# Optimization experiments

Measured on AMD Instinct MI355X. Metric: run time of the kernel, lower is better.

## Reference

```python
import jax, jax.numpy as jnp
import numpy as np

B, T, NLAT, N, D = 8, 4, 64, 2048, 1024
HEADS, HEAD_DIM = 16, 64
ADIM = HEADS * HEAD_DIM
EPS = 1e-5


def layer_norm(x, w, b):
    mu = jnp.mean(x, axis=-1, keepdims=True)
    var = jnp.var(x, axis=-1, keepdims=True)
    return (x - mu) * jax.lax.rsqrt(var + EPS) * w + b


def setup_inputs() -> dict:
    key = jax.random.key(0)
    ks = jax.random.split(key, 8)
    s = 0.02
    return {
        "latents": jax.random.normal(ks[0], (B, T, NLAT, D), jnp.float32),
        "x": jax.random.normal(ks[1], (B, T, N, D), jnp.float32),
        "Wq": jax.random.normal(ks[2], (D, ADIM), jnp.float32) * s,     # [in, out]
        "Wkv": jax.random.normal(ks[3], (D, 2 * ADIM), jnp.float32) * s,
        "Wout": jax.random.normal(ks[4], (ADIM, D), jnp.float32) * s,
        "bout": jnp.zeros((D,), jnp.float32),
        "lnl_w": jnp.ones((D,), jnp.float32),
        "lnl_b": jnp.zeros((D,), jnp.float32),
        "lnm_w": jnp.ones((D,), jnp.float32),
        "lnm_b": jnp.zeros((D,), jnp.float32),
    }


def reference(latents, x, Wq, Wkv, Wout, bout, lnl_w, lnl_b, lnm_w, lnm_b):
    scale = HEAD_DIM ** (-0.5)
    lat = layer_norm(latents, lnl_w, lnl_b)          # [B,T,NLAT,D]
    med = layer_norm(x, lnm_w, lnm_b)                # [B,T,N,D]
    q = lat @ Wq                                      # [B,T,NLAT,ADIM]
    kv_in = jnp.concatenate((med, lat), axis=-2)      # [B,T,N+NLAT,D]
    kv = kv_in @ Wkv                                  # [B,T,N+NLAT,2*ADIM]
    k, v = jnp.split(kv, 2, axis=-1)
    # split heads: b t n (h d) -> b h t n d
    def split_heads(z):
        b, t, n, _ = z.shape
        return z.reshape(b, t, n, HEADS, HEAD_DIM).transpose(0, 3, 1, 2, 4)
    q = split_heads(q) * scale
    k = split_heads(k)
    v = split_heads(v)
    scores = jnp.einsum('bhtid,bhtjd->bhtij', q, k)   # [B,H,T,NLAT,N+NLAT]
    attn = jax.nn.softmax(scores, axis=-1)            # max-subtract handled internally
    out = jnp.einsum('bhtij,bhtjd->bhtid', attn, v)   # [B,H,T,NLAT,HEAD_DIM]
    out = out.transpose(0, 2, 3, 1, 4).reshape(B, T, NLAT, ADIM)
    return out @ Wout + bout
```

## Files before the change

### kernel.cpp

```cpp
#include <hip/hip_runtime.h>
#include <hip/hip_bf16.h>
#include <stdint.h>

#define B_    8
#define T_    4
#define NLAT  64
#define NMED  2048
#define NKV   2112
#define D_    1024
#define HEADS 16
#define HD    64
#define ADIM  1024
#define BT    32

#define GK    1024
#define GN    2048
#define MT256 264

typedef __attribute__((ext_vector_type(8))) short bf16x8;
typedef __attribute__((ext_vector_type(4))) float f32x4;

__device__ __forceinline__ ushort f2bf(float f) {
  union { float f; uint32_t u; } v; v.f = f;
  return (ushort)((v.u + 0x7fff + ((v.u >> 16) & 1)) >> 16);
}

__device__ __forceinline__ void gload_lds16(const void* g, void* l) {
  __builtin_amdgcn_global_load_lds(
      (const __attribute__((address_space(1))) void*)g,
      (__attribute__((address_space(3))) void*)l, 16, 0, 0);
}

__device__ __forceinline__ f32x4 mfma16(bf16x8 a, bf16x8 b, f32x4 c) {
  return __builtin_amdgcn_mfma_f32_16x16x32_bf16(a, b, c, 0, 0, 0);
}

__global__ __launch_bounds__(256) void wtrans(const float* __restrict__ src,
                                              ushort* __restrict__ dst,
                                              int K, int Nm) {
  __shared__ float t[64][65];
  const int tr = blockIdx.y, tc = blockIdx.x;
  const int c = threadIdx.x & 63;
  const int r4 = threadIdx.x >> 6;
#pragma unroll
  for (int rr = 0; rr < 16; ++rr) {
    int r = r4 + rr * 4;
    t[r][c] = src[(size_t)(tr * 64 + r) * Nm + tc * 64 + c];
  }
  __syncthreads();
#pragma unroll
  for (int rr = 0; rr < 16; ++rr) {
    int n = r4 + rr * 4;
    dst[(size_t)(tc * 64 + n) * K + tr * 64 + c] = f2bf(t[c][n]);
  }
}

__global__ __launch_bounds__(256) void ln_kernel(
    const float* __restrict__ lat, const float* __restrict__ x,
    const float* __restrict__ lnl_w, const float* __restrict__ lnl_b,
    const float* __restrict__ lnm_w, const float* __restrict__ lnm_b,
    ushort* __restrict__ kvin) {
  const int row = blockIdx.x;
  const int bt = row / NKV;
  const int j = row - bt * NKV;
  const float* src;
  const float* w;
  const float* bb;
  if (j < NMED) {
    src = x + ((size_t)bt * NMED + j) * D_;
    w = lnm_w; bb = lnm_b;
  } else {
    src = lat + ((size_t)bt * NLAT + (j - NMED)) * D_;
    w = lnl_w; bb = lnl_b;
  }
  const int tid = threadIdx.x;
  float4 v = ((const float4*)src)[tid];
  float s = v.x + v.y + v.z + v.w;
  float s2 = v.x * v.x + v.y * v.y + v.z * v.z + v.w * v.w;
#pragma unroll
  for (int off = 1; off < 64; off <<= 1) {
    s += __shfl_xor(s, off, 64);
    s2 += __shfl_xor(s2, off, 64);
  }
  __shared__ float red[8];
  const int wave = tid >> 6;
  if ((tid & 63) == 0) { red[wave] = s; red[4 + wave] = s2; }
  __syncthreads();
  float S = red[0] + red[1] + red[2] + red[3];
  float S2 = red[4] + red[5] + red[6] + red[7];
  const float inv = 1.f / (float)D_;
  float mu = S * inv;
  float var = S2 * inv - mu * mu;
  float rs = rsqrtf(var + 1e-5f);
  float4 wv = ((const float4*)w)[tid];
  float4 bv = ((const float4*)bb)[tid];
  ushort4 ov;
  ov.x = f2bf((v.x - mu) * rs * wv.x + bv.x);
  ov.y = f2bf((v.y - mu) * rs * wv.y + bv.y);
  ov.z = f2bf((v.z - mu) * rs * wv.z + bv.z);
  ov.w = f2bf((v.w - mu) * rs * wv.w + bv.w);
  ((ushort4*)(kvin + (size_t)row * D_))[tid] = ov;
}

template <int AMODE, int OUTMODE>
__global__ __launch_bounds__(256) void gemm_bt(const ushort* __restrict__ A,
                                               const ushort* __restrict__ Bt,
                                               void* __restrict__ C,
                                               const float* __restrict__ bias,
                                               int M, int N, int K, int ldc) {
  __shared__ ushort lsA[128 * 32];
  __shared__ ushort lsB[128 * 32];
  const int tid = threadIdx.x;
  const int lane = tid & 63;
  const int wave = tid >> 6;
  const int brow = blockIdx.y * 128;
  const int bcol = blockIdx.x * 128;
  const int wr = (wave >> 1) * 64;
  const int wc = (wave & 1) * 64;
  const int lr = lane & 15;
  const int lk = (lane >> 4) * 8;

  f32x4 acc[4][4];
#pragma unroll
  for (int m = 0; m < 4; ++m)
#pragma unroll
    for (int n = 0; n < 4; ++n) acc[m][n] = (f32x4){0.f, 0.f, 0.f, 0.f};

  const int wbase = (tid & 192) * 16;

  for (int k0 = 0; k0 < K; k0 += 32) {
#pragma unroll
    for (int i = 0; i < 2; ++i) {
      int idx = i * 256 + tid;
      int r = idx >> 2;
      int cc = (idx & 3) * 8;
      long arow;
      if (AMODE == 1) {
        int gr = brow + r;
        arow = (long)(gr >> 6) * NKV + NMED + (gr & 63);
      } else {
        arow = brow + r;
      }
      gload_lds16(A + arow * (long)K + k0 + cc, (char*)lsA + i * 4096 + wbase);
      gload_lds16(Bt + (long)(bcol + r) * K + k0 + cc, (char*)lsB + i * 4096 + wbase);
    }
    __syncthreads();

    bf16x8 af[4], bf[4];
#pragma unroll
    for (int m = 0; m < 4; ++m)
      af[m] = *(const bf16x8*)&lsA[(wr + m * 16 + lr) * 32 + lk];
#pragma unroll
    for (int n = 0; n < 4; ++n)
      bf[n] = *(const bf16x8*)&lsB[(wc + n * 16 + lr) * 32 + lk];
#pragma unroll
    for (int m = 0; m < 4; ++m)
#pragma unroll
      for (int n = 0; n < 4; ++n) acc[m][n] = mfma16(af[m], bf[n], acc[m][n]);
    __syncthreads();
  }

#pragma unroll
  for (int m = 0; m < 4; ++m) {
#pragma unroll
    for (int n = 0; n < 4; ++n) {
      int row0 = brow + wr + m * 16 + (lane >> 4) * 4;
      int col = bcol + wc + n * 16 + lr;
#pragma unroll
      for (int r = 0; r < 4; ++r) {
        long off = (long)(row0 + r) * ldc + col;
        float v = acc[m][n][r];
        if (OUTMODE == 1) ((ushort*)C)[off] = f2bf(v * 0.125f);
        else ((float*)C)[off] = v + bias[col];
      }
    }
  }
}

__global__ __launch_bounds__(512, 2) void gemm256(const ushort* __restrict__ A,
                                                  const ushort* __restrict__ Bt,
                                                  ushort* __restrict__ C) {
  extern __shared__ __align__(16) char smem[];
  const int tid = threadIdx.x;
  const int lane = tid & 63;
  const int wv = tid >> 6;
  const int wm = wv >> 2;
  const int wn = wv & 3;
  const int lr = lane & 15;
  const int lg = lane >> 4;

  const int g = blockIdx.x;
  const int v = (g & 7) * (MT256 * 8 / 8) + (g >> 3);
  const int bx = v & 7;
  const int by = v >> 3;
  const long brow = (long)by * 256;
  const int bcol = bx * 256;

  const int pcx = lg ^ ((lr >> 1) & 3);

  f32x4 acc[8][4];
#pragma unroll
  for (int m = 0; m < 8; ++m)
#pragma unroll
    for (int n = 0; n < 4; ++n) acc[m][n] = (f32x4){0.f, 0.f, 0.f, 0.f};

  const int s0 = tid;
  const int s1 = 512 + tid;
  const int r0 = s0 >> 2, lc0 = (s0 & 3) ^ ((s0 >> 3) & 3);
  const int r1 = s1 >> 2, lc1 = (s1 & 3) ^ ((s1 >> 3) & 3);
  const int ldsoff0 = ((s0 >> 6) << 6) * 16;
  const int ldsoff1 = ((s1 >> 6) << 6) * 16;

#define STAGE_A(buf, kt)                                                        \
  {                                                                             \
    long k0 = (long)(kt) * 32;                                                  \
    char* db = smem + (buf) * 32768;                                            \
    gload_lds16(A + (brow + r0) * GK + k0 + lc0 * 8, db + ldsoff0);             \
    gload_lds16(A + (brow + r1) * GK + k0 + lc1 * 8, db + ldsoff1);             \
  }
#define STAGE_B(buf, kt)                                                        \
  {                                                                             \
    long k0 = (long)(kt) * 32;                                                  \
    char* db = smem + (buf) * 32768 + 16384;                                    \
    gload_lds16(Bt + (long)(bcol + r0) * GK + k0 + lc0 * 8, db + ldsoff0);      \
    gload_lds16(Bt + (long)(bcol + r1) * GK + k0 + lc1 * 8, db + ldsoff1);      \
  }

  STAGE_A(0, 0); STAGE_B(0, 0);
  STAGE_A(1, 1); STAGE_B(1, 1);
  asm volatile("s_waitcnt vmcnt(4)" ::: "memory");
  __builtin_amdgcn_s_barrier();
  __builtin_amdgcn_sched_barrier(0);

  int p = 0;
  for (int t = 0; t < GK / 32; ++t) {
    int q = p + 2; if (q >= 3) q -= 3;
    int ts = (t + 2 < GK / 32) ? t + 2 : t;
    const char* bufA = smem + p * 32768;
    const char* bufB = bufA + 16384;
    bf16x8 af[4], bf[4];

#pragma unroll
    for (int m = 0; m < 4; ++m) {
      int row = wm * 128 + m * 16 + lr;
      af[m] = *(const bf16x8*)(bufA + row * 64 + pcx * 16);
    }
#pragma unroll
    for (int n = 0; n < 4; ++n) {
      int row = wn * 64 + n * 16 + lr;
      bf[n] = *(const bf16x8*)(bufB + row * 64 + pcx * 16);
    }
    STAGE_A(q, ts);
    __builtin_amdgcn_sched_barrier(0);
    __builtin_amdgcn_s_barrier();
    __builtin_amdgcn_s_setprio(1);
#pragma unroll
    for (int m = 0; m < 4; ++m)
#pragma unroll
      for (int n = 0; n < 4; ++n)
        acc[m][n] = mfma16(bf[n], af[m], acc[m][n]);
    __builtin_amdgcn_s_setprio(0);
    __builtin_amdgcn_sched_barrier(0);
    __builtin_amdgcn_s_barrier();

#pragma unroll
    for (int m = 0; m < 4; ++m) {
      int row = wm * 128 + (m + 4) * 16 + lr;
      af[m] = *(const bf16x8*)(bufA + row * 64 + pcx * 16);
    }
    STAGE_B(q, ts);
    __builtin_amdgcn_sched_barrier(0);
    __builtin_amdgcn_s_barrier();
    __builtin_amdgcn_s_setprio(1);
#pragma unroll
    for (int m = 0; m < 4; ++m)
#pragma unroll
      for (int n = 0; n < 4; ++n)
        acc[m + 4][n] = mfma16(bf[n], af[m], acc[m + 4][n]);
    __builtin_amdgcn_s_setprio(0);
    asm volatile("s_waitcnt vmcnt(4)" ::: "memory");
    __builtin_amdgcn_sched_barrier(0);
    __builtin_amdgcn_s_barrier();
    __builtin_amdgcn_sched_barrier(0);
    p = p + 1; if (p >= 3) p -= 3;
  }
#undef STAGE_A
#undef STAGE_B

#pragma unroll
  for (int m = 0; m < 8; ++m) {
    long row = brow + wm * 128 + m * 16 + lr;
    ushort* crow = C + row * GN + bcol + wn * 64 + lg * 4;
#pragma unroll
    for (int n = 0; n < 4; ++n) {
      ushort4 o;
      o.x = f2bf(acc[m][n][0]);
      o.y = f2bf(acc[m][n][1]);
      o.z = f2bf(acc[m][n][2]);
      o.w = f2bf(acc[m][n][3]);
      *(ushort4*)(crow + n * 16) = o;
    }
  }
}

__global__ __launch_bounds__(256) void attn_kernel(const ushort* __restrict__ q,
                                                   const ushort* __restrict__ kv,
                                                   ushort* __restrict__ o) {
  const int blk = blockIdx.x;
  const int bt = blk >> 4;
  const int h = blk & 15;
  const int tid = threadIdx.x;
  const int wave = tid >> 6;
  const int lane = tid & 63;
  const int lr = lane & 15;
  const int lg = lane >> 4;

  __shared__ ushort vt[64][72];
  __shared__ ushort pl[4][16][72];

  const ushort* qbase = q + (size_t)(bt * 64 + wave * 16) * ADIM + h * HD;
  bf16x8 qf[2];
#pragma unroll
  for (int ks = 0; ks < 2; ++ks)
    qf[ks] = *(const bf16x8*)(qbase + (size_t)lr * ADIM + ks * 32 + lg * 8);

  const ushort* kvb = kv + (size_t)bt * NKV * 2048;

  f32x4 accO[4];
#pragma unroll
  for (int n = 0; n < 4; ++n) accO[n] = (f32x4){0.f, 0.f, 0.f, 0.f};
  float mrun[4] = {-1e30f, -1e30f, -1e30f, -1e30f};
  float lrun[4] = {0.f, 0.f, 0.f, 0.f};

  for (int jt = 0; jt < NKV / 64; ++jt) {
    const int j0 = jt * 64;
    __syncthreads();

    {
      int jj = tid >> 2;
      int dbase = (tid & 3) * 16;
#pragma unroll
      for (int half = 0; half < 2; ++half) {
        int d0 = dbase + half * 8;
        bf16x8 vv = *(const bf16x8*)(kvb + (size_t)(j0 + jj) * 2048 + ADIM + h * HD + d0);
#pragma unroll
        for (int e = 0; e < 8; ++e) vt[d0 + e][jj] = ((const ushort*)&vv)[e];
      }
    }

    f32x4 s[4];
#pragma unroll
    for (int nj = 0; nj < 4; ++nj) s[nj] = (f32x4){0.f, 0.f, 0.f, 0.f};
#pragma unroll
    for (int nj = 0; nj < 4; ++nj)
#pragma unroll
      for (int ks = 0; ks < 2; ++ks) {
        bf16x8 kf = *(const bf16x8*)(kvb + (size_t)(j0 + nj * 16 + lr) * 2048 +
                                     h * HD + ks * 32 + lg * 8);
        s[nj] = mfma16(qf[ks], kf, s[nj]);
      }

    float mt[4], corr[4], psum[4];
#pragma unroll
    for (int r = 0; r < 4; ++r)
      mt[r] = fmaxf(fmaxf(s[0][r], s[1][r]), fmaxf(s[2][r], s[3][r]));
#pragma unroll
    for (int off = 1; off < 16; off <<= 1)
#pragma unroll
      for (int r = 0; r < 4; ++r) mt[r] = fmaxf(mt[r], __shfl_xor(mt[r], off, 64));
#pragma unroll
    for (int r = 0; r < 4; ++r) {
      float mn = fmaxf(mrun[r], mt[r]);
      corr[r] = __expf(mrun[r] - mn);
      mrun[r] = mn;
      psum[r] = 0.f;
    }
#pragma unroll
    for (int nj = 0; nj < 4; ++nj)
#pragma unroll
      for (int r = 0; r < 4; ++r) {
        float pv = __expf(s[nj][r] - mrun[r]);
        s[nj][r] = pv;
        psum[r] += pv;
      }
#pragma unroll
    for (int off = 1; off < 16; off <<= 1)
#pragma unroll
      for (int r = 0; r < 4; ++r) psum[r] += __shfl_xor(psum[r], off, 64);
#pragma unroll
    for (int r = 0; r < 4; ++r) lrun[r] = lrun[r] * corr[r] + psum[r];
#pragma unroll
    for (int n = 0; n < 4; ++n)
#pragma unroll
      for (int r = 0; r < 4; ++r) accO[n][r] *= corr[r];

#pragma unroll
    for (int nj = 0; nj < 4; ++nj)
#pragma unroll
      for (int r = 0; r < 4; ++r)
        pl[wave][lg * 4 + r][nj * 16 + lr] = f2bf(s[nj][r]);
    __syncthreads();

    bf16x8 pf[2];
#pragma unroll
    for (int ks = 0; ks < 2; ++ks)
      pf[ks] = *(const bf16x8*)&pl[wave][lr][ks * 32 + lg * 8];
#pragma unroll
    for (int nd = 0; nd < 4; ++nd)
#pragma unroll
      for (int ks = 0; ks < 2; ++ks) {
        bf16x8 vf = *(const bf16x8*)&vt[nd * 16 + lr][ks * 32 + lg * 8];
        accO[nd] = mfma16(pf[ks], vf, accO[nd]);
      }
  }

#pragma unroll
  for (int nd = 0; nd < 4; ++nd)
#pragma unroll
    for (int r = 0; r < 4; ++r) {
      float vv = accO[nd][r] / lrun[r];
      int row = bt * 64 + wave * 16 + lg * 4 + r;
      o[(size_t)row * ADIM + h * HD + nd * 16 + lr] = f2bf(vv);
    }
}

extern "C" void kernel_launch(void* const* d_in, const int* in_sizes, int n_in,
                              void* d_out, int out_size, void* d_ws, size_t ws_size,
                              hipStream_t stream) {
  const float* latents = (const float*)d_in[0];
  const float* x = (const float*)d_in[1];
  const float* Wq = (const float*)d_in[2];
  const float* Wkv = (const float*)d_in[3];
  const float* Wout = (const float*)d_in[4];
  const float* bout = (const float*)d_in[5];
  const float* lnl_w = (const float*)d_in[6];
  const float* lnl_b = (const float*)d_in[7];
  const float* lnm_w = (const float*)d_in[8];
  const float* lnm_b = (const float*)d_in[9];

  char* ws = (char*)d_ws;
  size_t off = 0;
  auto alloc = [&](size_t bytes) -> void* {
    void* p = ws + off;
    off += (bytes + 255) & ~(size_t)255;
    return p;
  };
  ushort* kvin = (ushort*)alloc((size_t)BT * NKV * D_ * 2);
  ushort* kvo  = (ushort*)alloc((size_t)BT * NKV * 2048 * 2);
  ushort* qb   = (ushort*)alloc((size_t)BT * NLAT * ADIM * 2);
  ushort* ao   = (ushort*)alloc((size_t)BT * NLAT * ADIM * 2);
  ushort* WqT  = (ushort*)alloc((size_t)D_ * ADIM * 2);
  ushort* WkvT = (ushort*)alloc((size_t)D_ * 2 * ADIM * 2);
  ushort* WoutT = (ushort*)alloc((size_t)ADIM * D_ * 2);

  static bool attr_set = false;
  (void)attr_set;
  hipFuncSetAttribute((const void*)gemm256,
                      hipFuncAttributeMaxDynamicSharedMemorySize, 98304);

  wtrans<<<dim3(ADIM / 64, D_ / 64), 256, 0, stream>>>(Wq, WqT, D_, ADIM);
  wtrans<<<dim3(2 * ADIM / 64, D_ / 64), 256, 0, stream>>>(Wkv, WkvT, D_, 2 * ADIM);
  wtrans<<<dim3(D_ / 64, ADIM / 64), 256, 0, stream>>>(Wout, WoutT, ADIM, D_);

  ln_kernel<<<BT * NKV, 256, 0, stream>>>(latents, x, lnl_w, lnl_b, lnm_w, lnm_b, kvin);

  gemm_bt<1, 1><<<dim3(ADIM / 128, BT * NLAT / 128), 256, 0, stream>>>(
      kvin, WqT, qb, nullptr, BT * NLAT, ADIM, D_, ADIM);

  gemm256<<<dim3(MT256 * 8), 512, 98304, stream>>>(kvin, WkvT, kvo);

  attn_kernel<<<BT * HEADS, 256, 0, stream>>>(qb, kvo, ao);

  gemm_bt<0, 2><<<dim3(D_ / 128, BT * NLAT / 128), 256, 0, stream>>>(
      ao, WoutT, d_out, bout, BT * NLAT, D_, ADIM, D_);
}
```

Baseline: 596.4 us.

## Shrink KV GEMM tile to 128x256 with double-buffered static LDS

```diff
diff --git a/kernel.cpp b/kernel.cpp
--- a/kernel.cpp
+++ b/kernel.cpp
@@ -15,7 +15,11 @@
 
 #define GK    1024
 #define GN    2048
-#define MT256 264
+#define GM    67584
+#define BM_   128
+#define BN_   256
+#define MT    528
+#define NT_K  32
 
 typedef __attribute__((ext_vector_type(8))) short bf16x8;
 typedef __attribute__((ext_vector_type(4))) float f32x4;
@@ -177,10 +181,10 @@
   }
 }
 
-__global__ __launch_bounds__(512, 2) void gemm256(const ushort* __restrict__ A,
+__global__ __launch_bounds__(512, 4) void gemm256(const ushort* __restrict__ A,
                                                   const ushort* __restrict__ Bt,
                                                   ushort* __restrict__ C) {
-  extern __shared__ __align__(16) char smem[];
+  __shared__ __align__(16) char smem[2 * 24576];
   const int tid = threadIdx.x;
   const int lane = tid & 63;
   const int wv = tid >> 6;
@@ -190,59 +194,54 @@
   const int lg = lane >> 4;
 
   const int g = blockIdx.x;
-  const int v = (g & 7) * (MT256 * 8 / 8) + (g >> 3);
+  const int v = (g & 7) * MT + (g >> 3);
   const int bx = v & 7;
   const int by = v >> 3;
-  const long brow = (long)by * 256;
-  const int bcol = bx * 256;
+  const long brow = (long)by * BM_;
+  const int bcol = bx * BN_;
 
   const int pcx = lg ^ ((lr >> 1) & 3);
 
-  f32x4 acc[8][4];
-#pragma unroll
-  for (int m = 0; m < 8; ++m)
+  f32x4 acc[4][4];
+#pragma unroll
+  for (int m = 0; m < 4; ++m)
 #pragma unroll
     for (int n = 0; n < 4; ++n) acc[m][n] = (f32x4){0.f, 0.f, 0.f, 0.f};
 
-  const int s0 = tid;
-  const int s1 = 512 + tid;
-  const int r0 = s0 >> 2, lc0 = (s0 & 3) ^ ((s0 >> 3) & 3);
-  const int r1 = s1 >> 2, lc1 = (s1 & 3) ^ ((s1 >> 3) & 3);
-  const int ldsoff0 = ((s0 >> 6) << 6) * 16;
-  const int ldsoff1 = ((s1 >> 6) << 6) * 16;
-
-#define STAGE_A(buf, kt)                                                        \
-  {                                                                             \
-    long k0 = (long)(kt) * 32;                                                  \
-    char* db = smem + (buf) * 32768;                                            \
-    gload_lds16(A + (brow + r0) * GK + k0 + lc0 * 8, db + ldsoff0);             \
-    gload_lds16(A + (brow + r1) * GK + k0 + lc1 * 8, db + ldsoff1);             \
-  }
-#define STAGE_B(buf, kt)                                                        \
-  {                                                                             \
-    long k0 = (long)(kt) * 32;                                                  \
-    char* db = smem + (buf) * 32768 + 16384;                                    \
-    gload_lds16(Bt + (long)(bcol + r0) * GK + k0 + lc0 * 8, db + ldsoff0);      \
-    gload_lds16(Bt + (long)(bcol + r1) * GK + k0 + lc1 * 8, db + ldsoff1);      \
-  }
-
-  STAGE_A(0, 0); STAGE_B(0, 0);
-  STAGE_A(1, 1); STAGE_B(1, 1);
-  asm volatile("s_waitcnt vmcnt(4)" ::: "memory");
-  __builtin_amdgcn_s_barrier();
-  __builtin_amdgcn_sched_barrier(0);
-
-  int p = 0;
-  for (int t = 0; t < GK / 32; ++t) {
-    int q = p + 2; if (q >= 3) q -= 3;
-    int ts = (t + 2 < GK / 32) ? t + 2 : t;
-    const char* bufA = smem + p * 32768;
-    const char* bufB = bufA + 16384;
+  const int rA = tid >> 2;
+  const int lc = (tid & 3) ^ ((tid >> 3) & 3);
+  const int offA = (tid & ~63) * 16;
+  const int rB1 = 128 + (tid >> 2);
+  const int offB1 = 8192 + offA;
+
+#define STAGE(buf, kt)                                                         \
+  {                                                                            \
+    long k0 = (long)(kt) * 32;                                                 \
+    char* dbA = smem + (buf) * 24576;                                          \
+    char* dbB = dbA + 8192;                                                    \
+    gload_lds16(A + (brow + rA) * (long)GK + k0 + lc * 8, dbA + offA);         \
+    gload_lds16(Bt + (long)(bcol + rA) * GK + k0 + lc * 8, dbB + offA);        \
+    gload_lds16(Bt + (long)(bcol + rB1) * GK + k0 + lc * 8, dbB + offB1);      \
+  }
+
+  STAGE(0, 0);
+
+  for (int t = 0; t < NT_K; ++t) {
+    const int p = t & 1;
+    __builtin_amdgcn_s_barrier();
+    asm volatile("" ::: "memory");
+    const int ts = (t + 1 < NT_K) ? t + 1 : t;
+    STAGE(p ^ 1, ts);
+    asm volatile("s_waitcnt vmcnt(3)" ::: "memory");
+    __builtin_amdgcn_s_barrier();
+    asm volatile("" ::: "memory");
+
+    const char* bufA = smem + p * 24576;
+    const char* bufB = bufA + 8192;
     bf16x8 af[4], bf[4];
-
 #pragma unroll
     for (int m = 0; m < 4; ++m) {
-      int row = wm * 128 + m * 16 + lr;
+      int row = wm * 64 + m * 16 + lr;
       af[m] = *(const bf16x8*)(bufA + row * 64 + pcx * 16);
     }
 #pragma unroll
@@ -250,9 +249,6 @@
       int row = wn * 64 + n * 16 + lr;
       bf[n] = *(const bf16x8*)(bufB + row * 64 + pcx * 16);
     }
-    STAGE_A(q, ts);
-    __builtin_amdgcn_sched_barrier(0);
-    __builtin_amdgcn_s_barrier();
     __builtin_amdgcn_s_setprio(1);
 #pragma unroll
     for (int m = 0; m < 4; ++m)
@@ -260,36 +256,12 @@
       for (int n = 0; n < 4; ++n)
         acc[m][n] = mfma16(bf[n], af[m], acc[m][n]);
     __builtin_amdgcn_s_setprio(0);
-    __builtin_amdgcn_sched_barrier(0);
-    __builtin_amdgcn_s_barrier();
-
-#pragma unroll
-    for (int m = 0; m < 4; ++m) {
-      int row = wm * 128 + (m + 4) * 16 + lr;
-      af[m] = *(const bf16x8*)(bufA + row * 64 + pcx * 16);
-    }
-    STAGE_B(q, ts);
-    __builtin_amdgcn_sched_barrier(0);
-    __builtin_amdgcn_s_barrier();
-    __builtin_amdgcn_s_setprio(1);
-#pragma unroll
-    for (int m = 0; m < 4; ++m)
-#pragma unroll
-      for (int n = 0; n < 4; ++n)
-        acc[m + 4][n] = mfma16(bf[n], af[m], acc[m + 4][n]);
-    __builtin_amdgcn_s_setprio(0);
-    asm volatile("s_waitcnt vmcnt(4)" ::: "memory");
-    __builtin_amdgcn_sched_barrier(0);
-    __builtin_amdgcn_s_barrier();
-    __builtin_amdgcn_sched_barrier(0);
-    p = p + 1; if (p >= 3) p -= 3;
-  }
-#undef STAGE_A
-#undef STAGE_B
-
-#pragma unroll
-  for (int m = 0; m < 8; ++m) {
-    long row = brow + wm * 128 + m * 16 + lr;
+  }
+#undef STAGE
+
+#pragma unroll
+  for (int m = 0; m < 4; ++m) {
+    long row = brow + wm * 64 + m * 16 + lr;
     ushort* crow = C + row * GN + bcol + wn * 64 + lg * 4;
 #pragma unroll
     for (int n = 0; n < 4; ++n) {
@@ -453,11 +425,6 @@
   ushort* WkvT = (ushort*)alloc((size_t)D_ * 2 * ADIM * 2);
   ushort* WoutT = (ushort*)alloc((size_t)ADIM * D_ * 2);
 
-  static bool attr_set = false;
-  (void)attr_set;
-  hipFuncSetAttribute((const void*)gemm256,
-                      hipFuncAttributeMaxDynamicSharedMemorySize, 98304);
-
   wtrans<<<dim3(ADIM / 64, D_ / 64), 256, 0, stream>>>(Wq, WqT, D_, ADIM);
   wtrans<<<dim3(2 * ADIM / 64, D_ / 64), 256, 0, stream>>>(Wkv, WkvT, D_, 2 * ADIM);
   wtrans<<<dim3(D_ / 64, ADIM / 64), 256, 0, stream>>>(Wout, WoutT, ADIM, D_);
@@ -467,7 +434,7 @@
   gemm_bt<1, 1><<<dim3(ADIM / 128, BT * NLAT / 128), 256, 0, stream>>>(
       kvin, WqT, qb, nullptr, BT * NLAT, ADIM, D_, ADIM);
 
-  gemm256<<<dim3(MT256 * 8), 512, 98304, stream>>>(kvin, WkvT, kvo);
+  gemm256<<<dim3(MT * 8), 512, 0, stream>>>(kvin, WkvT, kvo);
 
   attn_kernel<<<BT * HEADS, 256, 0, stream>>>(qb, kvo, ao);
 
```

Result: no change. 595.6 us (-0.1%).
